# Kernel tuning notes

Measured on AMD Instinct MI355X. Metric: run time of the kernel, lower is better.

The kernel has to match this reference:

```python
import jax, jax.numpy as jnp
import numpy as np

SOFTMAX_TEMP = 0.01  # config['networks']['matcher_block']['softmax_temp']
B, WINDOW, C, N, WIDTH = 2, 2, 64, 400, 256


def setup_inputs() -> dict:
    key = jax.random.key(0)
    k1, k2, k3 = jax.random.split(key, 3)
    BW = B * WINDOW
    keypoint_scores = jax.random.uniform(k1, (BW, 1, N), dtype=jnp.float32)
    keypoint_desc = jax.random.normal(k2, (BW, C, N), dtype=jnp.float32)
    desc_dense = jax.random.normal(k3, (BW, C, WIDTH, WIDTH), dtype=jnp.float32)
    # pairing indices exactly as built in SoftmaxRefMatcher.__init__
    tgt_ids, src_ids = [], []
    for b in range(B):
        for w in range(WINDOW - 1):
            for t in range(w + 1, WINDOW):
                src_ids.append(w + b * WINDOW)
                tgt_ids.append(t + b * WINDOW)
    return {
        "keypoint_scores": keypoint_scores,
        "keypoint_desc": keypoint_desc,
        "desc_dense": desc_dense,
        "tgt_ids": jnp.array(tgt_ids, dtype=jnp.int32),
        "src_ids": jnp.array(src_ids, dtype=jnp.int32),
    }


def _l2_normalize(x):
    # F.normalize(x, dim=1), eps=1e-12
    return x / jnp.maximum(jnp.linalg.norm(x, axis=1, keepdims=True), 1e-12)


def reference(keypoint_scores, keypoint_desc, desc_dense, tgt_ids, src_ids):
    BW, Cdim, H, W = desc_dense.shape
    HW = H * W
    # src_coords_dense: meshgrid('ij') -> coords[k] = (u=k%W, v=k//W)
    hw = jnp.arange(HW)
    coords = jnp.stack([(hw % W).astype(jnp.float32),
                        (hw // W).astype(jnp.float32)], axis=1)  # [HW, 2]

    src_desc = _l2_normalize(desc_dense.reshape(BW, Cdim, HW))[src_ids]  # [P, C, HW]
    tgt_desc = _l2_normalize(keypoint_desc)[tgt_ids]                     # [P, C, N]

    match_vals = jnp.einsum('pcn,pcm->pnm', tgt_desc, src_desc)          # [P, N, HW]
    soft_match = jax.nn.softmax(match_vals / SOFTMAX_TEMP, axis=2)
    pseudo_coords = jnp.einsum('pnm,mk->pnk', soft_match, coords)        # [P, N, 2]

    tgt_scores = keypoint_scores[tgt_ids]
    return pseudo_coords, tgt_scores, tgt_ids, src_ids
```

## Files before the change

kernel.cpp:

```cpp
#include <hip/hip_runtime.h>
#include <math.h>

#define NPAIR  2
#define KDIM   64
#define NKP    400
#define NTILE  28
#define HWPIX  65536
#define MREF   70.0f
#define LOG2E  1.44269504f

#define BFRAG_DW (NPAIR*NTILE*2*2*256)

using frag_ab = __attribute__((ext_vector_type(8))) short;
using f32x4   = __attribute__((ext_vector_type(4))) float;

__device__ __forceinline__ unsigned short f2bf(float f){
    unsigned u = __builtin_bit_cast(unsigned, f);
    u += 0x7fffu + ((u >> 16) & 1u);
    return (unsigned short)(u >> 16);
}
__device__ __forceinline__ float bf2f(unsigned short h){
    unsigned u = ((unsigned)h) << 16;
    return __builtin_bit_cast(float, u);
}
__device__ __forceinline__ void async16(unsigned* lds, const unsigned* g){
    __builtin_amdgcn_global_load_lds(
        (const __attribute__((address_space(1))) unsigned*)g,
        (__attribute__((address_space(3))) unsigned*)lds, 16, 0, 0);
}

__global__ __launch_bounds__(256) void prep_kernel(
    const float* __restrict__ ksc, const float* __restrict__ kd,
    const int* __restrict__ tgt_ids, const int* __restrict__ src_ids,
    unsigned* __restrict__ wsu, float* __restrict__ out)
{
    __shared__ float xs[KDIM][33];
    __shared__ float inv_s[32];
    int d = blockIdx.x, p = blockIdx.y, t = threadIdx.x;
    int tgt = tgt_ids[p];
    int nl = t & 31, c0 = t >> 5;
    #pragma unroll
    for (int cc = 0; cc < 8; ++cc){
        int c = cc*8 + c0;
        int n = d*32 + nl;
        xs[c][nl] = (n < NKP) ? kd[(tgt*KDIM + c)*NKP + n] : 0.f;
    }
    __syncthreads();
    if (t < 32){
        float s = 0.f;
        #pragma unroll
        for (int c = 0; c < KDIM; ++c){ float v = xs[c][t]; s = fmaf(v, v, s); }
        inv_s[t] = 1.f / fmaxf(sqrtf(s), 1e-12f);
    }
    __syncthreads();
    {
        int l = t & 63, rk = t >> 6;
        int rt = rk >> 1, ks = rk & 1;
        int cl = l & 15, g = l >> 4;
        int nloc = rt*16 + cl;
        float inv = inv_s[nloc];
        int k0 = ks*32 + g*8;
        unsigned hu[4], lu[4];
        #pragma unroll
        for (int j2 = 0; j2 < 4; ++j2){
            float xa = xs[k0 + 2*j2    ][nloc] * inv;
            float xb = xs[k0 + 2*j2 + 1][nloc] * inv;
            unsigned short ha = f2bf(xa), hb = f2bf(xb);
            unsigned short la = f2bf(xa - bf2f(ha)), lb = f2bf(xb - bf2f(hb));
            hu[j2] = (unsigned)ha | ((unsigned)hb << 16);
            lu[j2] = (unsigned)la | ((unsigned)lb << 16);
        }
        int nt = d*2 + rt;
        unsigned base = (unsigned)(((p*NTILE + nt)*2 + ks)*2)*256 + l*4;
        *(uint4*)&wsu[base]       = make_uint4(hu[0], hu[1], hu[2], hu[3]);
        *(uint4*)&wsu[base + 256] = make_uint4(lu[0], lu[1], lu[2], lu[3]);
    }
    if (t < 32){
        int n = d*32 + t;
        if (n < NKP) out[NPAIR*NKP*2 + p*NKP + n] = ksc[tgt*NKP + n];
    }
    if (d == 0 && t == 0){
        out[NPAIR*NKP*3 + p]         = (float)tgt;
        out[NPAIR*NKP*3 + NPAIR + p] = (float)src_ids[p];
    }
}

__global__ __launch_bounds__(256, 4) void match_kernel(
    const float* __restrict__ dd, const int* __restrict__ src_ids,
    const unsigned* __restrict__ wsu, float* __restrict__ part)
{
    __shared__ unsigned Bst[4][1024];
    __shared__ float invn_s[128];
    __shared__ float wp[4*NTILE*16*2];
    int mb = blockIdx.x, p = blockIdx.y, t = threadIdx.x;
    int w = t >> 6, l = t & 63;
    int cl = l & 15, g = l >> 4;
    int mloc0 = w*32;

    const unsigned* wBp = wsu + (unsigned)p*(NTILE*1024) + (unsigned)t*4;
    auto bload = [&](int nt){
        async16(&Bst[nt & 3][(unsigned)w*256], wBp + (unsigned)nt*1024);
    };

    bload(0); bload(1);

    const float* ap = dd + (size_t)src_ids[p]*KDIM*HWPIX + (size_t)mb*128
                    + (unsigned)(mloc0 + cl);
    uint4 Ac[2][4];
    #pragma unroll
    for (int mt = 0; mt < 2; ++mt){
        float ss = 0.f;
        #pragma unroll
        for (int ks = 0; ks < 2; ++ks){
            float v[8];
            #pragma unroll
            for (int j = 0; j < 8; ++j)
                v[j] = ap[(size_t)(ks*32 + g*8 + j)*HWPIX + mt*16];
            unsigned hq[4], lq[4];
            #pragma unroll
            for (int q = 0; q < 4; ++q){
                float a = v[2*q], b = v[2*q+1];
                ss = fmaf(a, a, ss);
                ss = fmaf(b, b, ss);
                unsigned ta = (__builtin_bit_cast(unsigned, a) + 0x8000u) & 0xFFFF0000u;
                unsigned tb = (__builtin_bit_cast(unsigned, b) + 0x8000u) & 0xFFFF0000u;
                float la = a - __builtin_bit_cast(float, ta);
                float lb = b - __builtin_bit_cast(float, tb);
                hq[q] = __builtin_amdgcn_perm(tb, ta, 0x07060302u);
                lq[q] = __builtin_amdgcn_perm(__builtin_bit_cast(unsigned, lb),
                                              __builtin_bit_cast(unsigned, la), 0x07060302u);
            }
            Ac[mt][ks*2 + 0] = make_uint4(hq[0], hq[1], hq[2], hq[3]);
            Ac[mt][ks*2 + 1] = make_uint4(lq[0], lq[1], lq[2], lq[3]);
        }
        ss += __shfl_xor(ss, 16);
        ss += __shfl_xor(ss, 32);
        if (g == 0)
            invn_s[mloc0 + mt*16 + cl] = (100.f*LOG2E) / fmaxf(sqrtf(ss), 1e-12f);
    }
    __syncthreads();

    const float mref2 = MREF * LOG2E;
    float invm8[2][4], ub2[2];
    #pragma unroll
    for (int mt = 0; mt < 2; ++mt){
        ub2[mt] = (float)(mloc0 + mt*16 + g*4);
        #pragma unroll
        for (int r = 0; r < 4; ++r)
            invm8[mt][r] = invn_s[mloc0 + mt*16 + g*4 + r];
    }

    f32x4 acc0[2], acc1[2];
    auto zacc = [&](f32x4* a){
        a[0] = (f32x4){0.f,0.f,0.f,0.f};
        a[1] = (f32x4){0.f,0.f,0.f,0.f};
    };
    auto unit = [&](int nt, f32x4* a2){
        const unsigned* Bb = &Bst[nt & 3][0];
        #pragma unroll
        for (int ks = 0; ks < 2; ++ks){
            frag_ab bH  = __builtin_bit_cast(frag_ab, *(const uint4*)&Bb[(ks*2+0)*256 + l*4]);
            frag_ab bL  = __builtin_bit_cast(frag_ab, *(const uint4*)&Bb[(ks*2+1)*256 + l*4]);
            frag_ab a0H = __builtin_bit_cast(frag_ab, Ac[0][ks*2]);
            frag_ab a0L = __builtin_bit_cast(frag_ab, Ac[0][ks*2 + 1]);
            frag_ab a1H = __builtin_bit_cast(frag_ab, Ac[1][ks*2]);
            frag_ab a1L = __builtin_bit_cast(frag_ab, Ac[1][ks*2 + 1]);
            a2[0] = __builtin_amdgcn_mfma_f32_16x16x32_bf16(a0H, bH, a2[0], 0, 0, 0);
            a2[1] = __builtin_amdgcn_mfma_f32_16x16x32_bf16(a1H, bH, a2[1], 0, 0, 0);
            a2[0] = __builtin_amdgcn_mfma_f32_16x16x32_bf16(a0H, bL, a2[0], 0, 0, 0);
            a2[1] = __builtin_amdgcn_mfma_f32_16x16x32_bf16(a1H, bL, a2[1], 0, 0, 0);
            a2[0] = __builtin_amdgcn_mfma_f32_16x16x32_bf16(a0L, bH, a2[0], 0, 0, 0);
            a2[1] = __builtin_amdgcn_mfma_f32_16x16x32_bf16(a1L, bH, a2[1], 0, 0, 0);
        }
    };
    auto epi = [&](const f32x4* a2, int nt){
        float Ssum = 0.f, Usum = 0.f;
        #pragma unroll
        for (int mt = 0; mt < 2; ++mt){
            float e0 = __builtin_amdgcn_exp2f(fmaf(a2[mt][0], invm8[mt][0], -mref2));
            float e1 = __builtin_amdgcn_exp2f(fmaf(a2[mt][1], invm8[mt][1], -mref2));
            float e2 = __builtin_amdgcn_exp2f(fmaf(a2[mt][2], invm8[mt][2], -mref2));
            float e3 = __builtin_amdgcn_exp2f(fmaf(a2[mt][3], invm8[mt][3], -mref2));
            float Sm = (e0 + e1) + (e2 + e3);
            float Um = fmaf(e2, 2.f, e1);
            Um = fmaf(e3, 3.f, Um);
            Um = fmaf(ub2[mt], Sm, Um);
            Ssum += Sm; Usum += Um;
        }
        Ssum += __shfl_xor(Ssum, 16); Usum += __shfl_xor(Usum, 16);
        Ssum += __shfl_xor(Ssum, 32); Usum += __shfl_xor(Usum, 32);
        if (l < 16)
            *(float2*)&wp[((unsigned)(w*NTILE + nt)*16 + (unsigned)l)*2] =
                make_float2(Ssum, Usum);
    };

    #pragma unroll 1
    for (int j = 0; j < 14; ++j){
        if (j < 13){ bload(2*j + 2); bload(2*j + 3); }
        zacc(acc0); unit(2*j,     acc0);
        zacc(acc1); unit(2*j + 1, acc1);
        epi(acc0, 2*j);
        epi(acc1, 2*j + 1);
        __syncthreads();
    }

    for (int idx = t; idx < NTILE*16; idx += 256){
        int nt = idx >> 4, cc = idx & 15;
        float S = 0.f, U = 0.f;
        #pragma unroll
        for (int ww = 0; ww < 4; ++ww){
            float2 q = *(const float2*)&wp[((unsigned)(ww*NTILE + nt)*16 + (unsigned)cc)*2];
            S += q.x; U += q.y;
        }
        *(float2*)&part[(((size_t)p*NTILE + nt)*512 + mb)*32 + cc*2] =
            make_float2(S, U);
    }
}

__global__ __launch_bounds__(256) void merge_kernel(
    const float* __restrict__ part, float* __restrict__ out)
{
    __shared__ float red[3][4][16];
    int nt = blockIdx.x, p = blockIdx.y, t = threadIdx.x;
    int j = t & 15, mb0 = t >> 4;
    const float* base = part + ((size_t)(p*NTILE + nt)*512)*32;
    float S = 0.f, U = 0.f, V = 0.f;
    #pragma unroll 4
    for (int k = 0; k < 32; ++k){
        int mbk = mb0 + k*16;
        float2 q = *(const float2*)&base[(mbk*16 + j)*2];
        S += q.x;
        U += q.y + (float)((mbk & 1)*128)*q.x;
        V = fmaf((float)(mbk >> 1), q.x, V);
    }
    S += __shfl_xor(S, 16); U += __shfl_xor(U, 16); V += __shfl_xor(V, 16);
    S += __shfl_xor(S, 32); U += __shfl_xor(U, 32); V += __shfl_xor(V, 32);
    int w = t >> 6, l = t & 63;
    if (l < 16){ red[0][w][j] = S; red[1][w][j] = U; red[2][w][j] = V; }
    __syncthreads();
    if (t < 16){
        float Sf = red[0][0][t] + red[0][1][t] + red[0][2][t] + red[0][3][t];
        float Uf = red[1][0][t] + red[1][1][t] + red[1][2][t] + red[1][3][t];
        float Vf = red[2][0][t] + red[2][1][t] + red[2][2][t] + red[2][3][t];
        int n = nt*16 + t;
        out[(p*NKP + n)*2 + 0] = Uf / Sf;
        out[(p*NKP + n)*2 + 1] = Vf / Sf;
    }
}

extern "C" void kernel_launch(void* const* d_in, const int* in_sizes, int n_in,
                              void* d_out, int out_size, void* d_ws, size_t ws_size,
                              hipStream_t stream)
{
    const float* ksc     = (const float*)d_in[0];
    const float* kd      = (const float*)d_in[1];
    const float* dd      = (const float*)d_in[2];
    const int*   tgt_ids = (const int*)d_in[3];
    const int*   src_ids = (const int*)d_in[4];
    float* out = (float*)d_out;
    unsigned* wsu = (unsigned*)d_ws;
    float* part = (float*)d_ws + BFRAG_DW;

    prep_kernel <<<dim3(14, NPAIR),  256, 0, stream>>>(ksc, kd, tgt_ids, src_ids, wsu, out);
    match_kernel<<<dim3(512, NPAIR), 256, 0, stream>>>(dd, src_ids, wsu, part);
    merge_kernel<<<dim3(25, NPAIR),  256, 0, stream>>>(part, out);
}
```

Measured before the change: 129.6 us.

## Load B fragments into registers and write per-wave partials directly to global

Drops the LDS staging of B fragments via global_load_lds and the block barriers. Each wave now double-buffers B tiles in registers, loaded straight from global/L2. Each wave also writes its own (S,U) partial sums to global memory, replacing the in-block LDS reduction. The merge kernel is changed to reduce 2048 per-wave partials instead of 512 per-block ones, with the coordinate offsets adjusted to match. This removes __syncthreads and LDS use, at the cost of 4x more partial-sum traffic and a longer merge loop.

```diff
diff --git a/kernel.cpp b/kernel.cpp
--- a/kernel.cpp
+++ b/kernel.cpp
@@ -22,11 +22,6 @@
 __device__ __forceinline__ float bf2f(unsigned short h){
     unsigned u = ((unsigned)h) << 16;
     return __builtin_bit_cast(float, u);
-}
-__device__ __forceinline__ void async16(unsigned* lds, const unsigned* g){
-    __builtin_amdgcn_global_load_lds(
-        (const __attribute__((address_space(1))) unsigned*)g,
-        (__attribute__((address_space(3))) unsigned*)lds, 16, 0, 0);
 }
 
 __global__ __launch_bounds__(256) void prep_kernel(
@@ -89,24 +84,22 @@
     const float* __restrict__ dd, const int* __restrict__ src_ids,
     const unsigned* __restrict__ wsu, float* __restrict__ part)
 {
-    __shared__ unsigned Bst[4][1024];
-    __shared__ float invn_s[128];
-    __shared__ float wp[4*NTILE*16*2];
     int mb = blockIdx.x, p = blockIdx.y, t = threadIdx.x;
     int w = t >> 6, l = t & 63;
     int cl = l & 15, g = l >> 4;
-    int mloc0 = w*32;
-
-    const unsigned* wBp = wsu + (unsigned)p*(NTILE*1024) + (unsigned)t*4;
-    auto bload = [&](int nt){
-        async16(&Bst[nt & 3][(unsigned)w*256], wBp + (unsigned)nt*1024);
-    };
-
-    bload(0); bload(1);
-
-    const float* ap = dd + (size_t)src_ids[p]*KDIM*HWPIX + (size_t)mb*128
-                    + (unsigned)(mloc0 + cl);
+    int wq = mb*4 + w;
+
+    const unsigned* wB = wsu + (unsigned)p*(NTILE*1024) + (unsigned)l*4;
+    uint4 Bb0[4], Bb1[4];
+    #pragma unroll
+    for (int k = 0; k < 4; ++k) Bb0[k] = *(const uint4*)(wB + k*256);
+    #pragma unroll
+    for (int k = 0; k < 4; ++k) Bb1[k] = *(const uint4*)(wB + 1024 + k*256);
+
+    const float* ap = dd + (size_t)src_ids[p]*KDIM*HWPIX
+                    + (size_t)wq*32 + (unsigned)cl;
     uint4 Ac[2][4];
+    float invt[2];
     #pragma unroll
     for (int mt = 0; mt < 2; ++mt){
         float ss = 0.f;
@@ -135,32 +128,30 @@
         }
         ss += __shfl_xor(ss, 16);
         ss += __shfl_xor(ss, 32);
-        if (g == 0)
-            invn_s[mloc0 + mt*16 + cl] = (100.f*LOG2E) / fmaxf(sqrtf(ss), 1e-12f);
-    }
-    __syncthreads();
-
+        invt[mt] = (100.f*LOG2E) / fmaxf(sqrtf(ss), 1e-12f);
+    }
     const float mref2 = MREF * LOG2E;
     float invm8[2][4], ub2[2];
     #pragma unroll
     for (int mt = 0; mt < 2; ++mt){
-        ub2[mt] = (float)(mloc0 + mt*16 + g*4);
+        ub2[mt] = (float)(mt*16 + g*4);
         #pragma unroll
         for (int r = 0; r < 4; ++r)
-            invm8[mt][r] = invn_s[mloc0 + mt*16 + g*4 + r];
+            invm8[mt][r] = __shfl(invt[mt], g*4 + r);
     }
 
     f32x4 acc0[2], acc1[2];
+    float* pb = part + (((size_t)p*NTILE*2048 + wq)*16 + (unsigned)(l & 15))*2;
+
     auto zacc = [&](f32x4* a){
         a[0] = (f32x4){0.f,0.f,0.f,0.f};
         a[1] = (f32x4){0.f,0.f,0.f,0.f};
     };
-    auto unit = [&](int nt, f32x4* a2){
-        const unsigned* Bb = &Bst[nt & 3][0];
+    auto unit = [&](const uint4* Bq, f32x4* a2){
         #pragma unroll
         for (int ks = 0; ks < 2; ++ks){
-            frag_ab bH  = __builtin_bit_cast(frag_ab, *(const uint4*)&Bb[(ks*2+0)*256 + l*4]);
-            frag_ab bL  = __builtin_bit_cast(frag_ab, *(const uint4*)&Bb[(ks*2+1)*256 + l*4]);
+            frag_ab bH  = __builtin_bit_cast(frag_ab, Bq[ks*2]);
+            frag_ab bL  = __builtin_bit_cast(frag_ab, Bq[ks*2 + 1]);
             frag_ab a0H = __builtin_bit_cast(frag_ab, Ac[0][ks*2]);
             frag_ab a0L = __builtin_bit_cast(frag_ab, Ac[0][ks*2 + 1]);
             frag_ab a1H = __builtin_bit_cast(frag_ab, Ac[1][ks*2]);
@@ -173,6 +164,11 @@
             a2[1] = __builtin_amdgcn_mfma_f32_16x16x32_bf16(a1L, bH, a2[1], 0, 0, 0);
         }
     };
+    auto loadB = [&](int nt, uint4* B){
+        const unsigned* q = wB + (unsigned)nt*1024;
+        #pragma unroll
+        for (int k = 0; k < 4; ++k) B[k] = *(const uint4*)(q + k*256);
+    };
     auto epi = [&](const f32x4* a2, int nt){
         float Ssum = 0.f, Usum = 0.f;
         #pragma unroll
@@ -190,31 +186,22 @@
         Ssum += __shfl_xor(Ssum, 16); Usum += __shfl_xor(Usum, 16);
         Ssum += __shfl_xor(Ssum, 32); Usum += __shfl_xor(Usum, 32);
         if (l < 16)
-            *(float2*)&wp[((unsigned)(w*NTILE + nt)*16 + (unsigned)l)*2] =
-                make_float2(Ssum, Usum);
-    };
-
+            *(float2*)&pb[(size_t)nt*65536] = make_float2(Ssum, Usum);
+    };
+
+    zacc(acc0); unit(Bb0, acc0);
     #pragma unroll 1
-    for (int j = 0; j < 14; ++j){
-        if (j < 13){ bload(2*j + 2); bload(2*j + 3); }
-        zacc(acc0); unit(2*j,     acc0);
-        zacc(acc1); unit(2*j + 1, acc1);
+    for (int j = 0; j < 13; ++j){
+        loadB(2*j + 2, Bb0);
+        zacc(acc1); unit(Bb1, acc1);
         epi(acc0, 2*j);
+        loadB(2*j + 3, Bb1);
+        zacc(acc0); unit(Bb0, acc0);
         epi(acc1, 2*j + 1);
-        __syncthreads();
-    }
-
-    for (int idx = t; idx < NTILE*16; idx += 256){
-        int nt = idx >> 4, cc = idx & 15;
-        float S = 0.f, U = 0.f;
-        #pragma unroll
-        for (int ww = 0; ww < 4; ++ww){
-            float2 q = *(const float2*)&wp[((unsigned)(ww*NTILE + nt)*16 + (unsigned)cc)*2];
-            S += q.x; U += q.y;
-        }
-        *(float2*)&part[(((size_t)p*NTILE + nt)*512 + mb)*32 + cc*2] =
-            make_float2(S, U);
-    }
+    }
+    zacc(acc1); unit(Bb1, acc1);
+    epi(acc0, 26);
+    epi(acc1, 27);
 }
 
 __global__ __launch_bounds__(256) void merge_kernel(
@@ -222,16 +209,16 @@
 {
     __shared__ float red[3][4][16];
     int nt = blockIdx.x, p = blockIdx.y, t = threadIdx.x;
-    int j = t & 15, mb0 = t >> 4;
-    const float* base = part + ((size_t)(p*NTILE + nt)*512)*32;
+    int j = t & 15, s = t >> 4;
+    const float* base = part + ((size_t)(p*NTILE + nt)*2048)*32;
     float S = 0.f, U = 0.f, V = 0.f;
     #pragma unroll 4
-    for (int k = 0; k < 32; ++k){
-        int mbk = mb0 + k*16;
-        float2 q = *(const float2*)&base[(mbk*16 + j)*2];
+    for (int k = 0; k < 128; ++k){
+        int wq = s + k*16;
+        float2 q = *(const float2*)&base[(size_t)wq*32 + j*2];
         S += q.x;
-        U += q.y + (float)((mbk & 1)*128)*q.x;
-        V = fmaf((float)(mbk >> 1), q.x, V);
+        U += q.y + (float)((wq & 7)*32)*q.x;
+        V = fmaf((float)(wq >> 3), q.x, V);
     }
     S += __shfl_xor(S, 16); U += __shfl_xor(U, 16); V += __shfl_xor(V, 16);
     S += __shfl_xor(S, 32); U += __shfl_xor(U, 32); V += __shfl_xor(V, 32);
```

Measured after the change: 136.3 us. 1.05x slower.
